# Optimization experiments

Measured on AMD Instinct MI355X. Metric: run time of the kernel, lower is better.

## Reference

```python
import jax, jax.numpy as jnp
import numpy as np

N = 50000   # nodes
D = 128     # hidden_dim == in_dim
H = 4       # heads
C = 32      # hidden_dim // heads
L = 3       # message_layers
ET = 640000 # temporal edges
EH = 320000 # host edges


def layer_norm(x, g, b, eps=1e-5):
    m = x.mean(-1, keepdims=True)
    v = ((x - m) ** 2).mean(-1, keepdims=True)
    return (x - m) / jnp.sqrt(v + eps) * g + b


def transformer_conv(h, src, dst, e_emb, Wq, bq, Wk, bk, Wv, bv, We, Ws, bs):
    # PyG TransformerConv, concat=True, root_weight=True, beta=False
    n = h.shape[0]
    q = (h @ Wq + bq).reshape(n, H, C)
    k = (h @ Wk + bk).reshape(n, H, C)
    v = (h @ Wv + bv).reshape(n, H, C)
    ee = (e_emb @ We).reshape(-1, H, C)          # lin_edge has no bias
    kj = k[src] + ee                              # [E,H,C]
    a = (q[dst] * kj).sum(-1) / np.sqrt(C)        # [E,H]
    amax = jax.ops.segment_max(a, dst, num_segments=n)
    amax = jnp.where(jnp.isfinite(amax), amax, 0.0)
    ex = jnp.exp(a - amax[dst])
    den = jax.ops.segment_sum(ex, dst, num_segments=n)
    alpha = ex / (den[dst] + 1e-16)               # segment softmax over in-edges of dst
    msg = (v[src] + ee) * alpha[..., None]        # [E,H,C]
    out = jax.ops.segment_sum(msg, dst, num_segments=n).reshape(n, H * C)
    return out + h @ Ws + bs                      # root/skip connection


def mlp_head(h, W1, b1, g, bt, W2, b2):
    z = jax.nn.silu(h @ W1 + b1)
    z = layer_norm(z, g, bt)
    return z @ W2 + b2


def setup_inputs() -> dict:
    key = jax.random.key(0)
    ks = iter(jax.random.split(key, 80))
    nrm = lambda shape: jax.random.normal(next(ks), shape, jnp.float32) * 0.05
    inp = {}
    inp['x'] = jax.random.normal(next(ks), (N, D), jnp.float32)
    inp['edge_index_temporal'] = jax.random.randint(next(ks), (2, ET), 0, N)
    inp['edge_index_host'] = jax.random.randint(next(ks), (2, EH), 0, N)
    inp['edge_attr_temporal'] = jax.random.uniform(next(ks), (ET, 1), jnp.float32)
    inp['edge_attr_host'] = jax.random.normal(next(ks), (EH, 3), jnp.float32)
    # edge encoders
    inp['W_tedge'] = nrm((1, 4)); inp['b_tedge'] = jnp.zeros(4)
    inp['W_hedge'] = nrm((3, 4)); inp['b_hedge'] = jnp.zeros(4)
    # stacked conv params [L, ...] for temporal (_t) and host (_h) convs
    for s in ('t', 'h'):
        inp[f'Wq_{s}'] = nrm((L, D, D)); inp[f'bq_{s}'] = jnp.zeros((L, D))
        inp[f'Wk_{s}'] = nrm((L, D, D)); inp[f'bk_{s}'] = jnp.zeros((L, D))
        inp[f'Wv_{s}'] = nrm((L, D, D)); inp[f'bv_{s}'] = jnp.zeros((L, D))
        inp[f'We_{s}'] = nrm((L, 4, D))
        inp[f'Ws_{s}'] = nrm((L, D, D)); inp[f'bs_{s}'] = jnp.zeros((L, D))
    inp['norm_g'] = jnp.ones((L, D)); inp['norm_b'] = jnp.zeros((L, D))
    inp['fg'] = jnp.ones(D); inp['fb'] = jnp.zeros(D)
    inp['dW1'] = nrm((D, D)); inp['db1'] = jnp.zeros(D)
    inp['dg'] = jnp.ones(D); inp['dbt'] = jnp.zeros(D)
    inp['dW2'] = nrm((D, 3)); inp['db2'] = jnp.zeros(3)
    inp['sW1'] = nrm((D, D)); inp['sb1'] = jnp.zeros(D)
    inp['sg'] = jnp.ones(D); inp['sbt'] = jnp.zeros(D)
    inp['sW2'] = nrm((D, 3)); inp['sb2'] = jnp.zeros(3)
    return inp


def reference(x, edge_index_temporal, edge_index_host, edge_attr_temporal, edge_attr_host,
              W_tedge, b_tedge, W_hedge, b_hedge,
              Wq_t, bq_t, Wk_t, bk_t, Wv_t, bv_t, We_t, Ws_t, bs_t,
              Wq_h, bq_h, Wk_h, bk_h, Wv_h, bv_h, We_h, Ws_h, bs_h,
              norm_g, norm_b, fg, fb,
              dW1, db1, dg, dbt, dW2, db2,
              sW1, sb1, sg, sbt, sW2, sb2):
    te = edge_attr_temporal @ W_tedge + b_tedge   # [ET, edge_dim]
    he = edge_attr_host @ W_hedge + b_hedge       # [EH, edge_dim]
    st, dt_ = edge_index_temporal[0], edge_index_temporal[1]
    sh, dh = edge_index_host[0], edge_index_host[1]
    h = x
    for l in range(L):
        t_out = transformer_conv(h, st, dt_, te, Wq_t[l], bq_t[l], Wk_t[l], bk_t[l],
                                 Wv_t[l], bv_t[l], We_t[l], Ws_t[l], bs_t[l])
        h_out = transformer_conv(h, sh, dh, he, Wq_h[l], bq_h[l], Wk_h[l], bk_h[l],
                                 Wv_h[l], bv_h[l], We_h[l], Ws_h[l], bs_h[l])
        combined = jax.nn.silu(layer_norm(t_out + h_out, norm_g[l], norm_b[l]))
        h = h + combined  # residual (shapes match since in_dim == hidden_dim)
    h = layer_norm(h, fg, fb)
    drift = mlp_head(h, dW1, db1, dg, dbt, dW2, db2)
    diff = mlp_head(h, sW1, sb1, sg, sbt, sW2, sb2)
    return drift, diff
```

## Files before the change

### kernel.cpp

```cpp
#include <hip/hip_runtime.h>
#include <math.h>

#define NN 50000
#define DD 128
#define ET_N 640000
#define EH_N 320000
#define NL 3

static inline int cdiv(int a, int b){ return (a+b-1)/b; }

typedef __attribute__((ext_vector_type(8))) short short8;
typedef __attribute__((ext_vector_type(4))) float f32x4;

__device__ float   g_h [(size_t)NN*DD];
__device__ unsigned short g_hb[(size_t)NN*DD];
__device__ unsigned short g_Wb[(size_t)NL*8*DD*DD];
__device__ float   g_Q [2][(size_t)NN*DD];
__device__ float   g_S [2][(size_t)NN*DD];
__device__ ushort2 g_KV[2][(size_t)NN*DD];
__device__ float   g_to[(size_t)NN*DD];
__device__ float   g_ho[(size_t)NN*DD];
__device__ int     g_cnt[2][NN];
__device__ int     g_cur[2][NN];
__device__ int     g_rs [2][NN+1];
__device__ int     g_srcc[2][ET_N];
__device__ float   g_ta[ET_N];
__device__ float4  g_ha[EH_N];

__device__ inline unsigned short f2bf(float f){
  unsigned u = __float_as_uint(f);
  unsigned r = (u + 0x7fffu + ((u>>16)&1u)) >> 16;
  return (unsigned short)r;
}
__device__ inline float bf2f(unsigned short s){
  return __uint_as_float(((unsigned)s)<<16);
}
__device__ inline float bf_lo(unsigned u){ return __uint_as_float(u<<16); }
__device__ inline float bf_hi(unsigned u){ return __uint_as_float(u & 0xffff0000u); }

__global__ void k_copy_h(const float* __restrict__ x){
  int i = blockIdx.x*256 + threadIdx.x;
  if (i < NN*DD/4){
    float4 v = reinterpret_cast<const float4*>(x)[i];
    reinterpret_cast<float4*>(g_h)[i] = v;
    ushort4 b; b.x=f2bf(v.x); b.y=f2bf(v.y); b.z=f2bf(v.z); b.w=f2bf(v.w);
    reinterpret_cast<ushort4*>(g_hb)[i] = b;
  }
}

__global__ void k_zero_cnt(){
  int i = blockIdx.x*256 + threadIdx.x;
  if (i < NN) g_cnt[blockIdx.y][i] = 0;
}

struct WPtrs { const float* W[24]; };
__global__ __launch_bounds__(256) void k_cvtw(WPtrs wp){
  int mat = blockIdx.y;
  const float* W = wp.W[mat];
  int e = blockIdx.x*256 + threadIdx.x;
  int n = e >> 7, k = e & 127;
  g_Wb[(size_t)mat*DD*DD + e] = f2bf(W[k*DD+n]);
}

__global__ void k_hist(const int* __restrict__ dstT, const int* __restrict__ dstH){
  int which = blockIdx.y;
  int E = which ? EH_N : ET_N;
  const int* dst = which ? dstH : dstT;
  int e = blockIdx.x*256+threadIdx.x;
  if (e<E) atomicAdd(&g_cnt[which][dst[e]], 1);
}

__global__ __launch_bounds__(1024) void k_scan(){
  int which = blockIdx.y;
  int* row_start = g_rs[which];
  const int* cnt = g_cnt[which];
  int* cur = g_cur[which];
  __shared__ int buf[1024];
  int tid = threadIdx.x;
  const int n = NN;
  int chunk = (n + 1023) >> 10;
  int start = tid*chunk; if (start>n) start=n;
  int end = start+chunk; if (end>n) end=n;
  int lsum=0;
  for (int i=start;i<end;++i) lsum += cnt[i];
  buf[tid]=lsum;
  __syncthreads();
  for (int off=1; off<1024; off<<=1){
    int t = (tid>=off)? buf[tid-off]:0;
    __syncthreads();
    buf[tid] += t;
    __syncthreads();
  }
  int run = buf[tid]-lsum;
  for (int i=start;i<end;++i){ row_start[i]=run; cur[i]=run; run += cnt[i]; }
  if (tid==1023) row_start[n]=run;
}

__global__ void k_scatter(const int* __restrict__ eit, const int* __restrict__ eih,
                          const float* __restrict__ attrT, const float* __restrict__ attrH){
  int which = blockIdx.y;
  int e = blockIdx.x*256+threadIdx.x;
  if (which==0){
    if (e>=ET_N) return;
    int src = eit[e], dst = eit[ET_N+e];
    int p = atomicAdd(&g_cur[0][dst],1);
    g_srcc[0][p]=src;
    g_ta[p]=attrT[e];
  } else {
    if (e>=EH_N) return;
    int src = eih[e], dst = eih[EH_N+e];
    int p = atomicAdd(&g_cur[1][dst],1);
    g_srcc[1][p]=src;
    g_ha[p]=make_float4(attrH[e*3+0],attrH[e*3+1],attrH[e*3+2],0.f);
  }
}

struct BiasP { const float* b[8]; };

__global__ __launch_bounds__(256) void k_gemm_mfma(int l, BiasP bp){
  __shared__ unsigned short lA[64*DD];
  __shared__ unsigned short lB[DD*DD];
  int conv = blockIdx.y;
  int setbase = l*8 + conv*4;
  int tid = threadIdx.x;
  int m0 = blockIdx.x*64;

#pragma unroll
  for (int p=0;p<4;++p){
    int c = tid + p*256;
    int row = c >> 4, col16 = c & 15;
    int grow = m0 + row;
    uint4 v = make_uint4(0,0,0,0);
    if (grow < NN) v = *reinterpret_cast<const uint4*>(&g_hb[(size_t)grow*DD + col16*8]);
    int off = (row*256 + col16*16) ^ ((row&7)<<4);
    *reinterpret_cast<uint4*>((char*)lA + off) = v;
  }

  int wave = tid >> 6, lane = tid & 63;
  int lrow = lane & 15, kg = lane >> 4;
  int n0w = wave*32;

  auto stageB = [&](const unsigned short* Wm){
#pragma unroll
    for (int p=0;p<8;++p){
      int c = tid + p*256;
      int row = c >> 4, col16 = c & 15;
      uint4 v = *reinterpret_cast<const uint4*>(&Wm[(size_t)row*DD + col16*8]);
      int off = (row*256 + col16*16) ^ ((row&7)<<4);
      *reinterpret_cast<uint4*>((char*)lB + off) = v;
    }
  };

  stageB(&g_Wb[(size_t)(setbase+0)*DD*DD]);
  __syncthreads();

  short8 a[4][4];
#pragma unroll
  for (int kk=0;kk<4;++kk){
    int kbyte = kk*64 + kg*16;
#pragma unroll
    for (int mi=0;mi<4;++mi){
      int row = mi*16 + lrow;
      int off = (row*256 + kbyte) ^ ((row&7)<<4);
      a[kk][mi] = *reinterpret_cast<const short8*>((char*)lA + off);
    }
  }

  auto computeC = [&](f32x4 (&acc)[4][2]){
#pragma unroll
    for (int mi=0;mi<4;++mi)
#pragma unroll
      for (int ni=0;ni<2;++ni) acc[mi][ni] = (f32x4){0.f,0.f,0.f,0.f};
#pragma unroll
    for (int kk=0;kk<4;++kk){
      int kbyte = kk*64 + kg*16;
      short8 b[2];
#pragma unroll
      for (int ni=0;ni<2;++ni){
        int n = n0w + ni*16 + lrow;
        int off = (n*256 + kbyte) ^ ((n&7)<<4);
        b[ni] = *reinterpret_cast<const short8*>((char*)lB + off);
      }
#pragma unroll
      for (int mi=0;mi<4;++mi)
#pragma unroll
        for (int ni=0;ni<2;++ni)
          acc[mi][ni] = __builtin_amdgcn_mfma_f32_16x16x32_bf16(a[kk][mi], b[ni], acc[mi][ni], 0,0,0);
    }
  };

  f32x4 acc[4][2], accK[4][2];

  computeC(acc);
  {
    const float* bias = bp.b[conv*4+0];
    float* op = g_Q[conv];
#pragma unroll
    for (int ni=0;ni<2;++ni){
      int col = n0w + ni*16 + lrow;
      float bs = bias[col];
#pragma unroll
      for (int mi=0;mi<4;++mi)
#pragma unroll
        for (int r=0;r<4;++r){
          int row = m0 + mi*16 + kg*4 + r;
          if (row < NN) op[(size_t)row*DD + col] = acc[mi][ni][r] + bs;
        }
    }
  }
  __syncthreads();
  stageB(&g_Wb[(size_t)(setbase+1)*DD*DD]);
  __syncthreads();
  computeC(accK);
  __syncthreads();
  stageB(&g_Wb[(size_t)(setbase+2)*DD*DD]);
  __syncthreads();
  computeC(acc);
  {
    const float* bK = bp.b[conv*4+1];
    const float* bV = bp.b[conv*4+2];
#pragma unroll
    for (int ni=0;ni<2;++ni){
      int col = n0w + ni*16 + lrow;
      float bk = bK[col], bv = bV[col];
#pragma unroll
      for (int mi=0;mi<4;++mi)
#pragma unroll
        for (int r=0;r<4;++r){
          int row = m0 + mi*16 + kg*4 + r;
          if (row < NN){
            ushort2 kv;
            kv.x = f2bf(accK[mi][ni][r] + bk);
            kv.y = f2bf(acc [mi][ni][r] + bv);
            g_KV[conv][(size_t)row*DD + col] = kv;
          }
        }
    }
  }
  __syncthreads();
  stageB(&g_Wb[(size_t)(setbase+3)*DD*DD]);
  __syncthreads();
  computeC(acc);
  {
    const float* bias = bp.b[conv*4+3];
    float* op = g_S[conv];
#pragma unroll
    for (int ni=0;ni<2;++ni){
      int col = n0w + ni*16 + lrow;
      float bs = bias[col];
#pragma unroll
      for (int mi=0;mi<4;++mi)
#pragma unroll
        for (int r=0;r<4;++r){
          int row = m0 + mi*16 + kg*4 + r;
          if (row < NN) op[(size_t)row*DD + col] = acc[mi][ni][r] + bs;
        }
    }
  }
}

__device__ inline float waveRed(float v){
  v += __shfl_xor(v,32); v += __shfl_xor(v,16); v += __shfl_xor(v,8);
  v += __shfl_xor(v,4);  v += __shfl_xor(v,2);  v += __shfl_xor(v,1);
  return v;
}

__global__ __launch_bounds__(256) void k_agg(
    const float* __restrict__ WeT, const float* __restrict__ WeH,
    const float* __restrict__ Wt,  const float* __restrict__ bt4,
    const float* __restrict__ Wh,  const float* __restrict__ bh4){
  int conv = blockIdx.y;
  int wave = threadIdx.x >> 6;
  int lane = threadIdx.x & 63;
  int i = blockIdx.x*4 + wave;
  if (i >= NN) return;
  int g = lane >> 4;
  int t = lane & 15;
  int ch0 = t*8;

  const float* Qi = &g_Q[conv][(size_t)i*DD + ch0];
  float q[8];
  {
    float4 qA = *reinterpret_cast<const float4*>(Qi);
    float4 qB = *reinterpret_cast<const float4*>(Qi+4);
    q[0]=qA.x;q[1]=qA.y;q[2]=qA.z;q[3]=qA.w;q[4]=qB.x;q[5]=qB.y;q[6]=qB.z;q[7]=qB.w;
  }

  float cB[8], cA0[8], cA1[8], cA2[8];
#pragma unroll
  for (int r=0;r<8;++r){ cB[r]=0.f; cA0[r]=0.f; cA1[r]=0.f; cA2[r]=0.f; }
  if (conv==0){
#pragma unroll
    for (int j=0;j<4;++j){
      float4 wA = *reinterpret_cast<const float4*>(&WeT[j*DD+ch0]);
      float4 wB = *reinterpret_cast<const float4*>(&WeT[j*DD+ch0+4]);
      float w[8]={wA.x,wA.y,wA.z,wA.w,wB.x,wB.y,wB.z,wB.w};
      float bj=bt4[j], aj=Wt[j];
#pragma unroll
      for (int r=0;r<8;++r){ cB[r] += bj*w[r]; cA0[r] += aj*w[r]; }
    }
  } else {
#pragma unroll
    for (int j=0;j<4;++j){
      float4 wA = *reinterpret_cast<const float4*>(&WeH[j*DD+ch0]);
      float4 wB = *reinterpret_cast<const float4*>(&WeH[j*DD+ch0+4]);
      float w[8]={wA.x,wA.y,wA.z,wA.w,wB.x,wB.y,wB.z,wB.w};
      float a0=Wh[j], a1=Wh[4+j], a2=Wh[8+j], bj=bh4[j];
#pragma unroll
      for (int r=0;r<8;++r){ cA0[r]+=a0*w[r]; cA1[r]+=a1*w[r]; cA2[r]+=a2*w[r]; cB[r]+=bj*w[r]; }
    }
  }

  float qeB=0.f, qe0=0.f, qe1=0.f, qe2=0.f;
#pragma unroll
  for (int r=0;r<8;++r){ qeB += q[r]*cB[r]; qe0 += q[r]*cA0[r]; }
  qeB += __shfl_xor(qeB,1); qeB += __shfl_xor(qeB,2);
  qe0 += __shfl_xor(qe0,1); qe0 += __shfl_xor(qe0,2);
  if (conv==1){
#pragma unroll
    for (int r=0;r<8;++r){ qe1 += q[r]*cA1[r]; qe2 += q[r]*cA2[r]; }
    qe1 += __shfl_xor(qe1,1); qe1 += __shfl_xor(qe1,2);
    qe2 += __shfl_xor(qe2,1); qe2 += __shfl_xor(qe2,2);
  }

  const int* srcc = g_srcc[conv];
  const char* KVbase = (const char*)g_KV[conv];
  int beg=g_rs[conv][i], end=g_rs[conv][i+1];
  int cnt = end-beg;

  const float inv32 = 0.17677669529663687f;
  float den=0.f, x0=0.f, x1=0.f, x2=0.f;
  float ac[8];
#pragma unroll
  for (int r=0;r<8;++r) ac[r]=0.f;

  if (cnt>0){
    int nit = (cnt+3)>>2;
    int idx = beg + g;
    bool val = idx < end;
    int sidx = val ? idx : beg;
    int s = srcc[sidx];
    float4 at = make_float4(0.f,0.f,0.f,0.f);
    if (conv==0) at.x = g_ta[sidx]; else at = g_ha[sidx];
    const uint4* rp = reinterpret_cast<const uint4*>(KVbase + (size_t)s*512 + t*32);
    uint4 u0 = rp[0], u1 = rp[1];

    for (int it=0; it<nit; ++it){
      uint4 cu0=u0, cu1=u1; float4 ca=at; bool cval=val;
      if (it+1<nit){
        int nidx = beg + (it+1)*4 + g;
        val = nidx < end;
        int ns = srcc[val?nidx:beg];
        if (conv==0) at.x = g_ta[val?nidx:beg]; else at = g_ha[val?nidx:beg];
        rp = reinterpret_cast<const uint4*>(KVbase + (size_t)ns*512 + t*32);
        u0 = rp[0]; u1 = rp[1];
      }
      float k[8], v[8];
      k[0]=bf_lo(cu0.x); v[0]=bf_hi(cu0.x);
      k[1]=bf_lo(cu0.y); v[1]=bf_hi(cu0.y);
      k[2]=bf_lo(cu0.z); v[2]=bf_hi(cu0.z);
      k[3]=bf_lo(cu0.w); v[3]=bf_hi(cu0.w);
      k[4]=bf_lo(cu1.x); v[4]=bf_hi(cu1.x);
      k[5]=bf_lo(cu1.y); v[5]=bf_hi(cu1.y);
      k[6]=bf_lo(cu1.z); v[6]=bf_hi(cu1.z);
      k[7]=bf_lo(cu1.w); v[7]=bf_hi(cu1.w);
      float p = 0.f;
#pragma unroll
      for (int r=0;r<8;++r) p += q[r]*k[r];
      p += __shfl_xor(p,1); p += __shfl_xor(p,2);
      float lg = (conv==0) ? (p + qeB + ca.x*qe0)*inv32
                           : (p + ca.x*qe0 + ca.y*qe1 + ca.z*qe2 + qeB)*inv32;
      float e = cval ? __expf(lg) : 0.f;
      den += e;
#pragma unroll
      for (int r=0;r<8;++r) ac[r] += e*v[r];
      x0 += e*ca.x;
      if (conv==1){ x1 += e*ca.y; x2 += e*ca.z; }
    }
    den += __shfl_xor(den,16); den += __shfl_xor(den,32);
    x0  += __shfl_xor(x0,16);  x0  += __shfl_xor(x0,32);
    if (conv==1){
      x1 += __shfl_xor(x1,16); x1 += __shfl_xor(x1,32);
      x2 += __shfl_xor(x2,16); x2 += __shfl_xor(x2,32);
    }
#pragma unroll
    for (int r=0;r<8;++r){ ac[r] += __shfl_xor(ac[r],16); ac[r] += __shfl_xor(ac[r],32); }
  }

  if (g==0){
    float r8[8];
    if (cnt==0){
#pragma unroll
      for (int r=0;r<8;++r) r8[r]=0.f;
    } else {
      float id = 1.f/den;
      if (conv==0){
        float xm = x0*id;
#pragma unroll
        for (int r=0;r<8;++r) r8[r] = ac[r]*id + cB[r] + cA0[r]*xm;
      } else {
        float xm0=x0*id, xm1=x1*id, xm2=x2*id;
#pragma unroll
        for (int r=0;r<8;++r) r8[r] = ac[r]*id + cA0[r]*xm0 + cA1[r]*xm1 + cA2[r]*xm2 + cB[r];
      }
    }
    const float* Si = &g_S[conv][(size_t)i*DD + ch0];
    float4 sA = *reinterpret_cast<const float4*>(Si);
    float4 sB = *reinterpret_cast<const float4*>(Si+4);
    float* o = (conv ? g_ho : g_to) + (size_t)i*DD + ch0;
    float4 oA, oB;
    oA.x=r8[0]+sA.x; oA.y=r8[1]+sA.y; oA.z=r8[2]+sA.z; oA.w=r8[3]+sA.w;
    oB.x=r8[4]+sB.x; oB.y=r8[5]+sB.y; oB.z=r8[6]+sB.z; oB.w=r8[7]+sB.w;
    *reinterpret_cast<float4*>(o)   = oA;
    *reinterpret_cast<float4*>(o+4) = oB;
  }
}

__global__ __launch_bounds__(256) void k_combine(const float* __restrict__ g, const float* __restrict__ bt){
  int lane = threadIdx.x & 63;
  int node = blockIdx.x*4 + (threadIdx.x>>6);
  if (node>=NN) return;
  size_t i0 = (size_t)node*DD + lane, i1 = i0+64;
  float v0 = g_to[i0] + g_ho[i0];
  float v1 = g_to[i1] + g_ho[i1];
  float s = waveRed(v0+v1);
  float mean = s*(1.f/128.f);
  float d0=v0-mean, d1=v1-mean;
  float q = waveRed(d0*d0+d1*d1);
  float inv = 1.f/sqrtf(q*(1.f/128.f)+1e-5f);
  float c0 = d0*inv*g[lane]+bt[lane];
  float c1 = d1*inv*g[lane+64]+bt[lane+64];
  float h0 = g_h[i0] + c0/(1.f+__expf(-c0));
  float h1 = g_h[i1] + c1/(1.f+__expf(-c1));
  g_h[i0] = h0; g_h[i1] = h1;
  g_hb[i0] = f2bf(h0); g_hb[i1] = f2bf(h1);
}

__global__ __launch_bounds__(256) void k_finalln(const float* __restrict__ g, const float* __restrict__ b){
  int lane = threadIdx.x & 63;
  int node = blockIdx.x*4 + (threadIdx.x>>6);
  if (node>=NN) return;
  size_t i0 = (size_t)node*DD + lane, i1 = i0+64;
  float v0 = g_h[i0], v1 = g_h[i1];
  float s = waveRed(v0+v1);
  float mean = s*(1.f/128.f);
  float d0=v0-mean, d1=v1-mean;
  float q = waveRed(d0*d0+d1*d1);
  float inv = 1.f/sqrtf(q*(1.f/128.f)+1e-5f);
  g_h[i0]=d0*inv*g[lane]+b[lane];
  g_h[i1]=d1*inv*g[lane+64]+b[lane+64];
}

__global__ __launch_bounds__(128) void k_head(
      const float* __restrict__ W1, const float* __restrict__ b1,
      const float* __restrict__ g, const float* __restrict__ bt,
      const float* __restrict__ W2, const float* __restrict__ b2,
      float* __restrict__ out){
  int d = threadIdx.x;
  int wv = d >> 6;
  int i0 = blockIdx.x*8;
  const int n = NN;
  __shared__ float rows[8][DD];
  __shared__ float comb[2];
#pragma unroll
  for (int t=0;t<8;++t){
    int node = i0+t;
    rows[t][d] = (node<n)? g_h[(size_t)node*DD+d] : 0.f;
  }
  __syncthreads();
  float z[8];
  float b1d = b1[d];
#pragma unroll
  for (int t=0;t<8;++t) z[t]=b1d;
  for (int k=0;k<DD;++k){
    float w = W1[k*DD+d];
#pragma unroll
    for (int t=0;t<8;++t) z[t] += rows[t][k]*w;
  }
#pragma unroll
  for (int t=0;t<8;++t){ float v=z[t]; z[t] = v/(1.f+expf(-v)); }
  float gd=g[d], btd=bt[d];
  float w2a=W2[d*3+0], w2b=W2[d*3+1], w2c=W2[d*3+2];
  float b2a=b2[0], b2b=b2[1], b2c=b2[2];
  for (int t=0;t<8;++t){
    int node=i0+t;
    float zz=z[t];
    float s = waveRed(zz);
    if ((d&63)==0) comb[wv]=s;
    __syncthreads();
    float mean=(comb[0]+comb[1])*(1.f/128.f);
    __syncthreads();
    float dv=zz-mean;
    float q2 = waveRed(dv*dv);
    if ((d&63)==0) comb[wv]=q2;
    __syncthreads();
    float inv = 1.f/sqrtf((comb[0]+comb[1])*(1.f/128.f)+1e-5f);
    __syncthreads();
    float zn = dv*inv*gd+btd;
    float p0 = waveRed(zn*w2a);
    if ((d&63)==0) comb[wv]=p0;
    __syncthreads();
    float o0 = comb[0]+comb[1]+b2a;
    __syncthreads();
    float p1 = waveRed(zn*w2b);
    if ((d&63)==0) comb[wv]=p1;
    __syncthreads();
    float o1 = comb[0]+comb[1]+b2b;
    __syncthreads();
    float p2 = waveRed(zn*w2c);
    if ((d&63)==0) comb[wv]=p2;
    __syncthreads();
    float o2 = comb[0]+comb[1]+b2c;
    __syncthreads();
    if (d==0 && node<n){
      out[(size_t)node*3+0]=o0; out[(size_t)node*3+1]=o1; out[(size_t)node*3+2]=o2;
    }
  }
}

extern "C" void kernel_launch(void* const* d_in, const int* in_sizes, int n_in,
                              void* d_out, int out_size, void* d_ws, size_t ws_size,
                              hipStream_t stream){
  (void)in_sizes; (void)n_in; (void)out_size; (void)d_ws; (void)ws_size;
  const float* x    = (const float*)d_in[0];
  const int*   eit  = (const int*)d_in[1];
  const int*   eih  = (const int*)d_in[2];
  const float* eat  = (const float*)d_in[3];
  const float* eah  = (const float*)d_in[4];
  const float* W_te = (const float*)d_in[5];
  const float* b_te = (const float*)d_in[6];
  const float* W_he = (const float*)d_in[7];
  const float* b_he = (const float*)d_in[8];
  const float *Wq_t=(const float*)d_in[9],  *bq_t=(const float*)d_in[10];
  const float *Wk_t=(const float*)d_in[11], *bk_t=(const float*)d_in[12];
  const float *Wv_t=(const float*)d_in[13], *bv_t=(const float*)d_in[14];
  const float *We_t=(const float*)d_in[15];
  const float *Ws_t=(const float*)d_in[16], *bs_t=(const float*)d_in[17];
  const float *Wq_h=(const float*)d_in[18], *bq_h=(const float*)d_in[19];
  const float *Wk_h=(const float*)d_in[20], *bk_h=(const float*)d_in[21];
  const float *Wv_h=(const float*)d_in[22], *bv_h=(const float*)d_in[23];
  const float *We_h=(const float*)d_in[24];
  const float *Ws_h=(const float*)d_in[25], *bs_h=(const float*)d_in[26];
  const float *norm_g=(const float*)d_in[27], *norm_b=(const float*)d_in[28];
  const float *fg=(const float*)d_in[29], *fb=(const float*)d_in[30];
  const float *dW1=(const float*)d_in[31], *db1=(const float*)d_in[32];
  const float *dg=(const float*)d_in[33],  *dbt=(const float*)d_in[34];
  const float *dW2=(const float*)d_in[35], *db2=(const float*)d_in[36];
  const float *sW1=(const float*)d_in[37], *sb1=(const float*)d_in[38];
  const float *sg=(const float*)d_in[39],  *sbt=(const float*)d_in[40];
  const float *sW2=(const float*)d_in[41], *sb2=(const float*)d_in[42];
  float* outp = (float*)d_out;

  k_copy_h<<<cdiv(NN*DD/4,256),256,0,stream>>>(x);

  WPtrs wp;
  for (int l=0;l<NL;++l){
    wp.W[l*8+0]=Wq_t+(size_t)l*DD*DD; wp.W[l*8+1]=Wk_t+(size_t)l*DD*DD;
    wp.W[l*8+2]=Wv_t+(size_t)l*DD*DD; wp.W[l*8+3]=Ws_t+(size_t)l*DD*DD;
    wp.W[l*8+4]=Wq_h+(size_t)l*DD*DD; wp.W[l*8+5]=Wk_h+(size_t)l*DD*DD;
    wp.W[l*8+6]=Wv_h+(size_t)l*DD*DD; wp.W[l*8+7]=Ws_h+(size_t)l*DD*DD;
  }
  k_cvtw<<<dim3(64,24),256,0,stream>>>(wp);

  k_zero_cnt<<<dim3(cdiv(NN,256),2),256,0,stream>>>();
  k_hist<<<dim3(cdiv(ET_N,256),2),256,0,stream>>>(eit+ET_N, eih+EH_N);
  k_scan<<<dim3(1,2),1024,0,stream>>>();
  k_scatter<<<dim3(cdiv(ET_N,256),2),256,0,stream>>>(eit, eih, eat, eah);

  for (int l=0;l<NL;++l){
    BiasP bp;
    bp.b[0]=bq_t+(size_t)l*DD; bp.b[1]=bk_t+(size_t)l*DD;
    bp.b[2]=bv_t+(size_t)l*DD; bp.b[3]=bs_t+(size_t)l*DD;
    bp.b[4]=bq_h+(size_t)l*DD; bp.b[5]=bk_h+(size_t)l*DD;
    bp.b[6]=bv_h+(size_t)l*DD; bp.b[7]=bs_h+(size_t)l*DD;
    k_gemm_mfma<<<dim3(cdiv(NN,64),2),256,0,stream>>>(l, bp);
    k_agg<<<dim3(cdiv(NN,4),2),256,0,stream>>>(We_t+(size_t)l*4*DD, We_h+(size_t)l*4*DD,
                                               W_te, b_te, W_he, b_he);
    k_combine<<<cdiv(NN,4),256,0,stream>>>(norm_g+(size_t)l*DD, norm_b+(size_t)l*DD);
  }
  k_finalln<<<cdiv(NN,4),256,0,stream>>>(fg, fb);
  k_head<<<cdiv(NN,8),128,0,stream>>>(dW1, db1, dg, dbt, dW2, db2, outp);
  k_head<<<cdiv(NN,8),128,0,stream>>>(sW1, sb1, sg, sbt, sW2, sb2, outp+(size_t)NN*3);
}
```

Baseline: 1.241 ms.

## Precompute edge-encoder coefficients and per-node q·e terms outside aggregation

Edge-encoder products (W_edge·We and b_edge·We) are folded into per-layer channel coefficients once by a new kernel. A separate per-layer kernel computes each node's per-head q·coefficient dot products into a buffer that the aggregation kernel then reads. This removes the per-node We loads and reductions from the aggregation prologue and cuts its register pressure. The two MLP head launches are also merged into one grid. The cost is an extra kernel launch per layer and an extra read and write of the q·e buffer.

Result: faster. 1.177 ms (-5.1%).

```diff
diff --git a/kernel.cpp b/kernel.cpp
--- a/kernel.cpp
+++ b/kernel.cpp
@@ -26,6 +26,8 @@
 __device__ int     g_srcc[2][ET_N];
 __device__ float   g_ta[ET_N];
 __device__ float4  g_ha[EH_N];
+__device__ float   g_cf[NL][2][4][DD];
+__device__ float4  g_qe[2][(size_t)NN*4];
 
 __device__ inline unsigned short f2bf(float f){
   unsigned u = __float_as_uint(f);
@@ -60,6 +62,48 @@
   int e = blockIdx.x*256 + threadIdx.x;
   int n = e >> 7, k = e & 127;
   g_Wb[(size_t)mat*DD*DD + e] = f2bf(W[k*DD+n]);
+}
+
+__global__ void k_coef(const float* __restrict__ WeT, const float* __restrict__ WeH,
+                       const float* __restrict__ Wt,  const float* __restrict__ bt4,
+                       const float* __restrict__ Wh,  const float* __restrict__ bh4){
+  int ch = threadIdx.x;
+  int conv = blockIdx.x;
+  int l = blockIdx.y;
+  float a0=0.f,a1=0.f,a2=0.f,b=0.f;
+  if (conv==0){
+    const float* We = WeT + (size_t)l*4*DD;
+#pragma unroll
+    for (int j=0;j<4;++j){ float w=We[j*DD+ch]; a0 += Wt[j]*w; b += bt4[j]*w; }
+  } else {
+    const float* We = WeH + (size_t)l*4*DD;
+#pragma unroll
+    for (int j=0;j<4;++j){
+      float w=We[j*DD+ch];
+      a0 += Wh[j]*w; a1 += Wh[4+j]*w; a2 += Wh[8+j]*w; b += bh4[j]*w;
+    }
+  }
+  g_cf[l][conv][0][ch]=a0; g_cf[l][conv][1][ch]=a1;
+  g_cf[l][conv][2][ch]=a2; g_cf[l][conv][3][ch]=b;
+}
+
+__global__ __launch_bounds__(256) void k_qe(int l){
+  int conv = blockIdx.y;
+  int wave = threadIdx.x>>6, lane = threadIdx.x&63;
+  int i = blockIdx.x*4+wave; if (i>=NN) return;
+  int d0 = lane*2;
+  float2 q2 = *reinterpret_cast<const float2*>(&g_Q[conv][(size_t)i*DD+d0]);
+  const float (*cf)[DD] = g_cf[l][conv];
+  float s0 = q2.x*cf[0][d0] + q2.y*cf[0][d0+1];
+  float s1 = q2.x*cf[1][d0] + q2.y*cf[1][d0+1];
+  float s2 = q2.x*cf[2][d0] + q2.y*cf[2][d0+1];
+  float s3 = q2.x*cf[3][d0] + q2.y*cf[3][d0+1];
+#pragma unroll
+  for (int mk=1; mk<=8; mk<<=1){
+    s0 += __shfl_xor(s0,mk); s1 += __shfl_xor(s1,mk);
+    s2 += __shfl_xor(s2,mk); s3 += __shfl_xor(s3,mk);
+  }
+  if ((lane&15)==0) g_qe[conv][(size_t)i*4 + (lane>>4)] = make_float4(s0,s1,s2,s3);
 }
 
 __global__ void k_hist(const int* __restrict__ dstT, const int* __restrict__ dstH){
@@ -265,10 +309,7 @@
   return v;
 }
 
-__global__ __launch_bounds__(256) void k_agg(
-    const float* __restrict__ WeT, const float* __restrict__ WeH,
-    const float* __restrict__ Wt,  const float* __restrict__ bt4,
-    const float* __restrict__ Wh,  const float* __restrict__ bh4){
+__global__ __launch_bounds__(256) void k_agg(int l){
   int conv = blockIdx.y;
   int wave = threadIdx.x >> 6;
   int lane = threadIdx.x & 63;
@@ -285,43 +326,7 @@
     float4 qB = *reinterpret_cast<const float4*>(Qi+4);
     q[0]=qA.x;q[1]=qA.y;q[2]=qA.z;q[3]=qA.w;q[4]=qB.x;q[5]=qB.y;q[6]=qB.z;q[7]=qB.w;
   }
-
-  float cB[8], cA0[8], cA1[8], cA2[8];
-#pragma unroll
-  for (int r=0;r<8;++r){ cB[r]=0.f; cA0[r]=0.f; cA1[r]=0.f; cA2[r]=0.f; }
-  if (conv==0){
-#pragma unroll
-    for (int j=0;j<4;++j){
-      float4 wA = *reinterpret_cast<const float4*>(&WeT[j*DD+ch0]);
-      float4 wB = *reinterpret_cast<const float4*>(&WeT[j*DD+ch0+4]);
-      float w[8]={wA.x,wA.y,wA.z,wA.w,wB.x,wB.y,wB.z,wB.w};
-      float bj=bt4[j], aj=Wt[j];
-#pragma unroll
-      for (int r=0;r<8;++r){ cB[r] += bj*w[r]; cA0[r] += aj*w[r]; }
-    }
-  } else {
-#pragma unroll
-    for (int j=0;j<4;++j){
-      float4 wA = *reinterpret_cast<const float4*>(&WeH[j*DD+ch0]);
-      float4 wB = *reinterpret_cast<const float4*>(&WeH[j*DD+ch0+4]);
-      float w[8]={wA.x,wA.y,wA.z,wA.w,wB.x,wB.y,wB.z,wB.w};
-      float a0=Wh[j], a1=Wh[4+j], a2=Wh[8+j], bj=bh4[j];
-#pragma unroll
-      for (int r=0;r<8;++r){ cA0[r]+=a0*w[r]; cA1[r]+=a1*w[r]; cA2[r]+=a2*w[r]; cB[r]+=bj*w[r]; }
-    }
-  }
-
-  float qeB=0.f, qe0=0.f, qe1=0.f, qe2=0.f;
-#pragma unroll
-  for (int r=0;r<8;++r){ qeB += q[r]*cB[r]; qe0 += q[r]*cA0[r]; }
-  qeB += __shfl_xor(qeB,1); qeB += __shfl_xor(qeB,2);
-  qe0 += __shfl_xor(qe0,1); qe0 += __shfl_xor(qe0,2);
-  if (conv==1){
-#pragma unroll
-    for (int r=0;r<8;++r){ qe1 += q[r]*cA1[r]; qe2 += q[r]*cA2[r]; }
-    qe1 += __shfl_xor(qe1,1); qe1 += __shfl_xor(qe1,2);
-    qe2 += __shfl_xor(qe2,1); qe2 += __shfl_xor(qe2,2);
-  }
+  float4 qe = g_qe[conv][(size_t)i*4 + (t>>2)];
 
   const int* srcc = g_srcc[conv];
   const char* KVbase = (const char*)g_KV[conv];
@@ -368,8 +373,8 @@
 #pragma unroll
       for (int r=0;r<8;++r) p += q[r]*k[r];
       p += __shfl_xor(p,1); p += __shfl_xor(p,2);
-      float lg = (conv==0) ? (p + qeB + ca.x*qe0)*inv32
-                           : (p + ca.x*qe0 + ca.y*qe1 + ca.z*qe2 + qeB)*inv32;
+      float lg = (conv==0) ? (p + qe.w + ca.x*qe.x)*inv32
+                           : (p + ca.x*qe.x + ca.y*qe.y + ca.z*qe.z + qe.w)*inv32;
       float e = cval ? __expf(lg) : 0.f;
       den += e;
 #pragma unroll
@@ -388,6 +393,22 @@
   }
 
   if (g==0){
+    const float (*cf)[DD] = g_cf[l][conv];
+    float cA0[8], cA1[8], cA2[8], cB[8];
+    {
+      float4 a0A=*reinterpret_cast<const float4*>(&cf[0][ch0]);
+      float4 a0B=*reinterpret_cast<const float4*>(&cf[0][ch0+4]);
+      float4 a1A=*reinterpret_cast<const float4*>(&cf[1][ch0]);
+      float4 a1B=*reinterpret_cast<const float4*>(&cf[1][ch0+4]);
+      float4 a2A=*reinterpret_cast<const float4*>(&cf[2][ch0]);
+      float4 a2B=*reinterpret_cast<const float4*>(&cf[2][ch0+4]);
+      float4 bA =*reinterpret_cast<const float4*>(&cf[3][ch0]);
+      float4 bB =*reinterpret_cast<const float4*>(&cf[3][ch0+4]);
+      cA0[0]=a0A.x;cA0[1]=a0A.y;cA0[2]=a0A.z;cA0[3]=a0A.w;cA0[4]=a0B.x;cA0[5]=a0B.y;cA0[6]=a0B.z;cA0[7]=a0B.w;
+      cA1[0]=a1A.x;cA1[1]=a1A.y;cA1[2]=a1A.z;cA1[3]=a1A.w;cA1[4]=a1B.x;cA1[5]=a1B.y;cA1[6]=a1B.z;cA1[7]=a1B.w;
+      cA2[0]=a2A.x;cA2[1]=a2A.y;cA2[2]=a2A.z;cA2[3]=a2A.w;cA2[4]=a2B.x;cA2[5]=a2B.y;cA2[6]=a2B.z;cA2[7]=a2B.w;
+      cB[0]=bA.x;cB[1]=bA.y;cB[2]=bA.z;cB[3]=bA.w;cB[4]=bB.x;cB[5]=bB.y;cB[6]=bB.z;cB[7]=bB.w;
+    }
     float r8[8];
     if (cnt==0){
 #pragma unroll
@@ -451,11 +472,17 @@
   g_h[i1]=d1*inv*g[lane+64]+b[lane+64];
 }
 
-__global__ __launch_bounds__(128) void k_head(
-      const float* __restrict__ W1, const float* __restrict__ b1,
-      const float* __restrict__ g, const float* __restrict__ bt,
-      const float* __restrict__ W2, const float* __restrict__ b2,
-      float* __restrict__ out){
+struct HeadP { const float* W1; const float* b1; const float* g; const float* bt;
+               const float* W2; const float* b2; float* out; };
+__global__ __launch_bounds__(128) void k_head(HeadP h0, HeadP h1){
+  const HeadP hp = blockIdx.y ? h1 : h0;
+  const float* __restrict__ W1 = hp.W1;
+  const float* __restrict__ b1 = hp.b1;
+  const float* __restrict__ g  = hp.g;
+  const float* __restrict__ bt = hp.bt;
+  const float* __restrict__ W2 = hp.W2;
+  const float* __restrict__ b2 = hp.b2;
+  float* __restrict__ out = hp.out;
   int d = threadIdx.x;
   int wv = d >> 6;
   int i0 = blockIdx.x*8;
@@ -561,6 +588,7 @@
     wp.W[l*8+6]=Wv_h+(size_t)l*DD*DD; wp.W[l*8+7]=Ws_h+(size_t)l*DD*DD;
   }
   k_cvtw<<<dim3(64,24),256,0,stream>>>(wp);
+  k_coef<<<dim3(2,NL),128,0,stream>>>(We_t, We_h, W_te, b_te, W_he, b_he);
 
   k_zero_cnt<<<dim3(cdiv(NN,256),2),256,0,stream>>>();
   k_hist<<<dim3(cdiv(ET_N,256),2),256,0,stream>>>(eit+ET_N, eih+EH_N);
@@ -574,11 +602,13 @@
     bp.b[4]=bq_h+(size_t)l*DD; bp.b[5]=bk_h+(size_t)l*DD;
     bp.b[6]=bv_h+(size_t)l*DD; bp.b[7]=bs_h+(size_t)l*DD;
     k_gemm_mfma<<<dim3(cdiv(NN,64),2),256,0,stream>>>(l, bp);
-    k_agg<<<dim3(cdiv(NN,4),2),256,0,stream>>>(We_t+(size_t)l*4*DD, We_h+(size_t)l*4*DD,
-                                               W_te, b_te, W_he, b_he);
+    k_qe<<<dim3(cdiv(NN,4),2),256,0,stream>>>(l);
+    k_agg<<<dim3(cdiv(NN,4),2),256,0,stream>>>(l);
     k_combine<<<cdiv(NN,4),256,0,stream>>>(norm_g+(size_t)l*DD, norm_b+(size_t)l*DD);
   }
   k_finalln<<<cdiv(NN,4),256,0,stream>>>(fg, fb);
-  k_head<<<cdiv(NN,8),128,0,stream>>>(dW1, db1, dg, dbt, dW2, db2, outp);
-  k_head<<<cdiv(NN,8),128,0,stream>>>(sW1, sb1, sg, sbt, sW2, sb2, outp+(size_t)NN*3);
-}
+  HeadP hd, hs;
+  hd.W1=dW1; hd.b1=db1; hd.g=dg; hd.bt=dbt; hd.W2=dW2; hd.b2=db2; hd.out=outp;
+  hs.W1=sW1; hs.b1=sb1; hs.g=sg; hs.bt=sbt; hs.W2=sW2; hs.b2=sb2; hs.out=outp+(size_t)NN*3;
+  k_head<<<dim3(cdiv(NN,8),2),128,0,stream>>>(hd, hs);
+}
```
